# Kernel tuning notes

Measured on AMD Instinct MI355X. Metric: run time of the kernel, lower is better.

## Reference

```python
import jax, jax.numpy as jnp
import numpy as np

N, E = 50000, 800000
D_IN, D_HID, D_OUT = 128, 256, 128


def setup_inputs() -> dict:
    key = jax.random.key(0)
    k = jax.random.split(key, 7)
    x = jax.random.normal(k[0], (N, D_IN), dtype=jnp.float32)
    edge_src = jax.random.randint(k[1], (E,), 0, N, dtype=jnp.int32)
    edge_dst = jax.random.randint(k[2], (E,), 0, N, dtype=jnp.int32)
    s1 = 1.0 / np.sqrt(2 * D_IN)
    s2 = 1.0 / np.sqrt(2 * D_HID)
    W1 = jax.random.uniform(k[3], (2 * D_IN, D_HID), jnp.float32, -s1, s1)
    b1 = jax.random.uniform(k[4], (D_HID,), jnp.float32, -s1, s1)
    W2 = jax.random.uniform(k[5], (2 * D_HID, D_OUT), jnp.float32, -s2, s2)
    b2 = jax.random.uniform(k[6], (D_OUT,), jnp.float32, -s2, s2)
    return {"x": x, "edge_src": edge_src, "edge_dst": edge_dst,
            "W1": W1, "b1": b1, "W2": W2, "b2": b2}


def _sage_layer(h, edge_src, edge_dst, W, b, inv_deg):
    # mean-pool neighbor features: gather [E, D] then segment-sum to [N, D]
    msgs = h[edge_src]
    agg = jax.ops.segment_sum(msgs, edge_dst, num_segments=h.shape[0]) * inv_deg
    y = jnp.concatenate([h, agg], axis=1)  # [N, 2D]
    return y @ W + b


def reference(x, edge_src, edge_dst, W1, b1, W2, b2):
    n = x.shape[0]
    deg = jax.ops.segment_sum(jnp.ones_like(edge_dst, dtype=x.dtype), edge_dst,
                              num_segments=n)
    inv_deg = (1.0 / jnp.maximum(deg, 1.0))[:, None]  # isolated nodes -> zeros
    h = _sage_layer(x, edge_src, edge_dst, W1, b1, inv_deg)
    h = jax.nn.relu(h)
    # dropout is identity in eval mode
    h = _sage_layer(h, edge_src, edge_dst, W2, b2, inv_deg)
    return jax.nn.log_softmax(h, axis=1)
```

## Files before the change

### kernel.cpp

```cpp
#include <hip/hip_runtime.h>
#include <cstdint>
#include <cstddef>

typedef __attribute__((ext_vector_type(8))) short bf16x8;
typedef __attribute__((ext_vector_type(4))) float f32x4;
typedef __attribute__((ext_vector_type(2))) float f32x2;

__device__ inline short bf16_rne(float f) {
  unsigned u = __builtin_bit_cast(unsigned, f);
  u += 0x7fff + ((u >> 16) & 1);
  return (short)(u >> 16);
}

__device__ inline float bf16lo(unsigned v) { return __builtin_bit_cast(float, v << 16); }
__device__ inline float bf16hi(unsigned v) { return __builtin_bit_cast(float, v & 0xffff0000u); }

__device__ inline unsigned pack2(float a, float b) {
  return ((unsigned)(unsigned short)bf16_rne(a)) | (((unsigned)(unsigned short)bf16_rne(b)) << 16);
}


__global__ __launch_bounds__(256) void prep_kernel(const float* __restrict__ W1,
                                                   const float* __restrict__ W2,
                                                   const float* __restrict__ b2,
                                                   const float* __restrict__ x,
                                                   short* __restrict__ B1p,
                                                   short* __restrict__ B2p,
                                                   float* __restrict__ bias2,
                                                   unsigned* __restrict__ A1u,
                                                   unsigned* __restrict__ xf8, int nquads,
                                                   int* __restrict__ counters, int NB) {
  int b = blockIdx.x;
  int tid = threadIdx.x;
  int nqb = (nquads + 32 + 255) >> 8;
  if (b < 512) {
    int mode = b >> 8;
    int idx = (b & 255) * 256 + tid;
    int j = idx & 7;
    int L = (idx >> 3) & 63;
    int nt = (idx >> 9) & 15;
    int kb = idx >> 13;
    int k = kb * 32 + (L >> 4) * 8 + j;
    int n = nt * 16 + (L & 15);
    if (mode == 0) {
      B1p[idx] = bf16_rne(W1[(size_t)k * 256 + n]);
    } else {
      float v = (n < 128) ? W2[(size_t)k * 128 + n] : W2[(size_t)(256 + k) * 128 + (n - 128)];
      B2p[idx] = bf16_rne(v);
    }
  } else if (b == 512) {
    bias2[tid] = (tid < 128) ? b2[tid] : 0.0f;
  } else if (b < 513 + nqb) {
    int idx = (b - 513) * 256 + tid;
    if (idx < nquads) {
      int n = idx >> 5, q = idx & 31;
      float4 v = ((const float4*)x)[idx];
      ((uint2*)A1u)[(size_t)n * 64 + q] = make_uint2(pack2(v.x, v.y), pack2(v.z, v.w));
      int pk = __builtin_amdgcn_cvt_pk_fp8_f32(v.x, v.y, 0, false);
      pk = __builtin_amdgcn_cvt_pk_fp8_f32(v.z, v.w, pk, true);
      xf8[(size_t)n * 32 + q] = (unsigned)pk;
    } else if (idx < nquads + 32) {
      int n = idx >> 5, q = idx & 31;
      ((uint2*)A1u)[(size_t)n * 64 + q] = make_uint2(0u, 0u);
      xf8[(size_t)n * 32 + q] = 0u;
    }
  } else {
    for (int t = tid; t < NB; t += 256) counters[t] = 0;
  }
}

__global__ __launch_bounds__(256) void bucket_scatter(const int* __restrict__ src,
                                                      const int* __restrict__ dst, int E, int EPB,
                                                      int* __restrict__ counters, int NB,
                                                      int SLACK, unsigned* __restrict__ bedge) {
  __shared__ int h[512];
  __shared__ int base[512];
  int tid = threadIdx.x;
  for (int t = tid; t < NB; t += 256) h[t] = 0;
  __syncthreads();
  int start = blockIdx.x * EPB, end = min(E, start + EPB);
  for (int i = start + tid; i < end; i += 256) atomicAdd(&h[((unsigned)dst[i]) >> 7], 1);
  __syncthreads();
  for (int t = tid; t < NB; t += 256) {
    int c = h[t];
    base[t] = (c > 0) ? atomicAdd(&counters[t], c) : 0;
    h[t] = 0;
  }
  __syncthreads();
  for (int i = start + tid; i < end; i += 256) {
    unsigned d = (unsigned)dst[i];
    unsigned bk = d >> 7;
    int p = base[bk] + atomicAdd(&h[bk], 1);
    bedge[(size_t)bk * SLACK + p] = ((d & 127u) << 24) | (unsigned)src[i];
  }
}

__global__ __launch_bounds__(256) void build_csr(const unsigned* __restrict__ bedge,
                                                 const int* __restrict__ counters,
                                                 int NB, int SLACK, int N,
                                                 int* __restrict__ offsets,
                                                 int* __restrict__ oend,
                                                 float* __restrict__ inv_deg,
                                                 int* __restrict__ ssrc) {
  __shared__ int buf[128];
  __shared__ int cur[128];
  __shared__ int lim[128];
  int b = blockIdx.x, tid = threadIdx.x;
  int cntE = counters[b];
  int rb = b * SLACK;
  if (tid < 128) buf[tid] = 0;
  __syncthreads();
  for (int i = tid; i < cntE; i += 256) atomicAdd(&buf[bedge[(size_t)rb + i] >> 24], 1);
  __syncthreads();
  int cnt = (tid < 128) ? buf[tid] : 0;
  int pcnt = min((cnt + 3) & ~3, 64);
  if (tid < 128) buf[tid] = pcnt;
  __syncthreads();
  #pragma unroll
  for (int off = 1; off < 128; off <<= 1) {
    int t = (tid >= off && tid < 128) ? buf[tid - off] : 0;
    __syncthreads();
    if (tid < 128) buf[tid] += t;
    __syncthreads();
  }
  int excl = 0;
  if (tid < 128) {
    excl = buf[tid] - pcnt;
    int node = (b << 7) + tid;
    if (node < N) {
      offsets[node] = rb + excl;
      oend[node]    = rb + excl + pcnt;
      inv_deg[node] = 1.0f / fmaxf((float)cnt, 1.0f);
    }
  }
  __syncthreads();
  if (tid < 128) {
    cur[tid] = rb + excl;
    lim[tid] = rb + excl + pcnt;
  }
  __syncthreads();
  for (int i = tid; i < cntE; i += 256) {
    unsigned e2 = bedge[(size_t)rb + i];
    int nd = e2 >> 24;
    int p = atomicAdd(&cur[nd], 1);
    if (p < lim[nd]) ssrc[p] = (int)(e2 & 0xFFFFFFu);
  }
  __syncthreads();
  if (tid < 128) {
    int base0 = rb + excl;
    for (int p2 = cnt; p2 < pcnt; ++p2) ssrc[base0 + p2] = N;
  }
}

#define CVT8(U, A0, A1, A2, A3, A4, A5, A6, A7)                                        \
  {                                                                                    \
    f32x2 p_, q_;                                                                      \
    p_ = __builtin_amdgcn_cvt_pk_f32_fp8((U).x, false);                                \
    q_ = __builtin_amdgcn_cvt_pk_f32_fp8((U).x, true);                                 \
    A0 += p_[0]; A1 += p_[1]; A2 += q_[0]; A3 += q_[1];                                \
    p_ = __builtin_amdgcn_cvt_pk_f32_fp8((U).y, false);                                \
    q_ = __builtin_amdgcn_cvt_pk_f32_fp8((U).y, true);                                 \
    A4 += p_[0]; A5 += p_[1]; A6 += q_[0]; A7 += q_[1];                                \
  }

__global__ __launch_bounds__(256) void agg1_kernel(const uint2* __restrict__ X8,
                                                   const int* __restrict__ offsets,
                                                   const int* __restrict__ oend,
                                                   const int* __restrict__ ssrc,
                                                   const float* __restrict__ inv_deg,
                                                   uint4* __restrict__ A1q, int N) {
  int node = blockIdx.x * 4 + (threadIdx.x >> 6);
  if (node >= N) return;
  int lane = threadIdx.x & 63;
  int g = lane >> 4;
  int l = lane & 15;
  int s = offsets[node];
  int nq = (oend[node] - s) >> 2;
  int sv = ssrc[s + lane];
  float a0=0.f,a1=0.f,a2=0.f,a3=0.f,a4=0.f,a5=0.f,a6=0.f,a7=0.f;
  int q = 0;
  for (; q + 4 <= nq; q += 4) {
    int sA = __shfl(sv, (q + 0) * 4 + g, 64);
    int sB = __shfl(sv, (q + 1) * 4 + g, 64);
    int sC = __shfl(sv, (q + 2) * 4 + g, 64);
    int sD = __shfl(sv, (q + 3) * 4 + g, 64);
    uint2 u = X8[((size_t)(unsigned)sA << 4) + l];
    uint2 v = X8[((size_t)(unsigned)sB << 4) + l];
    uint2 w = X8[((size_t)(unsigned)sC << 4) + l];
    uint2 z = X8[((size_t)(unsigned)sD << 4) + l];
    CVT8(u, a0,a1,a2,a3,a4,a5,a6,a7);
    CVT8(v, a0,a1,a2,a3,a4,a5,a6,a7);
    CVT8(w, a0,a1,a2,a3,a4,a5,a6,a7);
    CVT8(z, a0,a1,a2,a3,a4,a5,a6,a7);
  }
  for (; q < nq; ++q) {
    int sA = __shfl(sv, q * 4 + g, 64);
    uint2 u = X8[((size_t)(unsigned)sA << 4) + l];
    CVT8(u, a0,a1,a2,a3,a4,a5,a6,a7);
  }
  a0 += __shfl_xor(a0,16,64); a0 += __shfl_xor(a0,32,64);
  a1 += __shfl_xor(a1,16,64); a1 += __shfl_xor(a1,32,64);
  a2 += __shfl_xor(a2,16,64); a2 += __shfl_xor(a2,32,64);
  a3 += __shfl_xor(a3,16,64); a3 += __shfl_xor(a3,32,64);
  a4 += __shfl_xor(a4,16,64); a4 += __shfl_xor(a4,32,64);
  a5 += __shfl_xor(a5,16,64); a5 += __shfl_xor(a5,32,64);
  a6 += __shfl_xor(a6,16,64); a6 += __shfl_xor(a6,32,64);
  a7 += __shfl_xor(a7,16,64); a7 += __shfl_xor(a7,32,64);
  if (g == 0) {
    float id = inv_deg[node];
    A1q[((size_t)node << 5) + 16 + l] =
        make_uint4(pack2(a0 * id, a1 * id), pack2(a2 * id, a3 * id),
                   pack2(a4 * id, a5 * id), pack2(a6 * id, a7 * id));
  }
}

__global__ __launch_bounds__(512, 2) void gemm_fused(const short* __restrict__ A,
                                                     const short* __restrict__ B1,
                                                     const short* __restrict__ B2,
                                                     const float* __restrict__ bias1,
                                                     const float* __restrict__ bias2,
                                                     short* __restrict__ utop,
                                                     unsigned char* __restrict__ t2,
                                                     int S, int Nvalid) {
  __shared__ char hls[2 * 16 * 512];
  int tid = threadIdx.x;
  int wv = tid >> 6;
  int lane = tid & 63;
  int role = wv >> 2;
  int w = wv & 3;
  int rowf = lane & 15;
  int g = lane >> 4;

  const short* Bp = role ? B2 : B1;
  const float* bias = role ? bias2 : bias1;

  bf16x8 breg[8][4];
  #pragma unroll
  for (int kb = 0; kb < 8; ++kb)
    #pragma unroll
    for (int j = 0; j < 4; ++j)
      breg[kb][j] = *(const bf16x8*)(Bp + ((size_t)((kb * 16 + w * 4 + j) * 64 + lane)) * 8);

  f32x4 bj[4];
  #pragma unroll
  for (int j = 0; j < 4; ++j)
    bj[j] = *(const f32x4*)(bias + w * 64 + j * 16 + g * 4);

  for (int i = 0;; ++i) {
    int sP = blockIdx.x + i * gridDim.x;
    int sC = blockIdx.x + (i - 1) * gridDim.x;
    bool anyP = sP < S;
    bool anyC = (i > 0) && (sC < S);
    if (!anyP && !anyC) break;

    if (role == 0) {
      if (anyP) {
        int row0 = sP * 16;
        const short* Arow = A + (size_t)(row0 + rowf) * 256 + g * 8;
        bf16x8 afr[8];
        #pragma unroll
        for (int kb = 0; kb < 8; ++kb) afr[kb] = *(const bf16x8*)(Arow + kb * 32);
        f32x4 acc[4];
        #pragma unroll
        for (int j = 0; j < 4; ++j) acc[j] = (f32x4)(0.0f);
        __builtin_amdgcn_s_setprio(1);
        #pragma unroll
        for (int kb = 0; kb < 8; ++kb)
          #pragma unroll
          for (int j = 0; j < 4; ++j)
            acc[j] = __builtin_amdgcn_mfma_f32_16x16x32_bf16(breg[kb][j], afr[kb], acc[j], 0, 0, 0);
        __builtin_amdgcn_s_setprio(0);
        int buf = (i & 1) * 8192;
        #pragma unroll
        for (int j = 0; j < 4; ++j) {
          float v0 = fmaxf(acc[j][0] + bj[j][0], 0.0f);
          float v1 = fmaxf(acc[j][1] + bj[j][1], 0.0f);
          float v2 = fmaxf(acc[j][2] + bj[j][2], 0.0f);
          float v3 = fmaxf(acc[j][3] + bj[j][3], 0.0f);
          int c0 = w * 64 + j * 16 + g * 4;
          int chunk = c0 >> 3;
          int swz = chunk ^ rowf ^ ((chunk & 1) << 4);
          *(uint2*)(hls + buf + rowf * 512 + swz * 16 + ((c0 & 4) << 1)) =
              make_uint2(pack2(v0, v1), pack2(v2, v3));
        }
      }
    } else {
      if (anyC) {
        int buf = ((i - 1) & 1) * 8192;
        bf16x8 afr[8];
        #pragma unroll
        for (int kb = 0; kb < 8; ++kb) {
          int chunk = kb * 4 + g;
          int swz = chunk ^ rowf ^ ((chunk & 1) << 4);
          afr[kb] = *(const bf16x8*)(hls + buf + rowf * 512 + swz * 16);
        }
        f32x4 acc[4];
        #pragma unroll
        for (int j = 0; j < 4; ++j) acc[j] = (f32x4)(0.0f);
        __builtin_amdgcn_s_setprio(1);
        #pragma unroll
        for (int kb = 0; kb < 8; ++kb)
          #pragma unroll
          for (int j = 0; j < 4; ++j)
            acc[j] = __builtin_amdgcn_mfma_f32_16x16x32_bf16(breg[kb][j], afr[kb], acc[j], 0, 0, 0);
        __builtin_amdgcn_s_setprio(0);
        int row = sC * 16 + rowf;
        bool live = row < Nvalid;
        #pragma unroll
        for (int j = 0; j < 4; ++j) {
          float v0 = live ? acc[j][0] + bj[j][0] : 0.0f;
          float v1 = live ? acc[j][1] + bj[j][1] : 0.0f;
          float v2 = live ? acc[j][2] + bj[j][2] : 0.0f;
          float v3 = live ? acc[j][3] + bj[j][3] : 0.0f;
          int c0 = w * 64 + j * 16 + g * 4;
          if (w < 2) {
            *(uint2*)(utop + (size_t)row * 128 + c0) = make_uint2(pack2(v0, v1), pack2(v2, v3));
          } else {
            int pk = __builtin_amdgcn_cvt_pk_fp8_f32(v0, v1, 0, false);
            pk = __builtin_amdgcn_cvt_pk_fp8_f32(v2, v3, pk, true);
            *(unsigned*)(t2 + (size_t)row * 128 + (c0 - 128)) = (unsigned)pk;
          }
        }
      }
    }
    __syncthreads();
  }
}

__global__ __launch_bounds__(256) void final_kernel(const uint4* __restrict__ utopq,
                                                    const uint2* __restrict__ T2,
                                                    const int* __restrict__ offsets,
                                                    const int* __restrict__ oend,
                                                    const int* __restrict__ ssrc,
                                                    const float* __restrict__ inv_deg,
                                                    float4* __restrict__ out4, int N) {
  int node = blockIdx.x * 4 + (threadIdx.x >> 6);
  if (node >= N) return;
  int lane = threadIdx.x & 63;
  int g = lane >> 4;
  int l = lane & 15;
  int s = offsets[node];
  int nq = (oend[node] - s) >> 2;
  int sv = ssrc[s + lane];
  float a0=0.f,a1=0.f,a2=0.f,a3=0.f,a4=0.f,a5=0.f,a6=0.f,a7=0.f;
  int q = 0;
  for (; q + 4 <= nq; q += 4) {
    int sA = __shfl(sv, (q + 0) * 4 + g, 64);
    int sB = __shfl(sv, (q + 1) * 4 + g, 64);
    int sC = __shfl(sv, (q + 2) * 4 + g, 64);
    int sD = __shfl(sv, (q + 3) * 4 + g, 64);
    uint2 u = T2[((size_t)(unsigned)sA << 4) + l];
    uint2 v = T2[((size_t)(unsigned)sB << 4) + l];
    uint2 w = T2[((size_t)(unsigned)sC << 4) + l];
    uint2 z = T2[((size_t)(unsigned)sD << 4) + l];
    CVT8(u, a0,a1,a2,a3,a4,a5,a6,a7);
    CVT8(v, a0,a1,a2,a3,a4,a5,a6,a7);
    CVT8(w, a0,a1,a2,a3,a4,a5,a6,a7);
    CVT8(z, a0,a1,a2,a3,a4,a5,a6,a7);
  }
  for (; q < nq; ++q) {
    int sA = __shfl(sv, q * 4 + g, 64);
    uint2 u = T2[((size_t)(unsigned)sA << 4) + l];
    CVT8(u, a0,a1,a2,a3,a4,a5,a6,a7);
  }
  a0 += __shfl_xor(a0,16,64); a0 += __shfl_xor(a0,32,64);
  a1 += __shfl_xor(a1,16,64); a1 += __shfl_xor(a1,32,64);
  a2 += __shfl_xor(a2,16,64); a2 += __shfl_xor(a2,32,64);
  a3 += __shfl_xor(a3,16,64); a3 += __shfl_xor(a3,32,64);
  a4 += __shfl_xor(a4,16,64); a4 += __shfl_xor(a4,32,64);
  a5 += __shfl_xor(a5,16,64); a5 += __shfl_xor(a5,32,64);
  a6 += __shfl_xor(a6,16,64); a6 += __shfl_xor(a6,32,64);
  a7 += __shfl_xor(a7,16,64); a7 += __shfl_xor(a7,32,64);
  if (g == 0) {
    float id = inv_deg[node];
    uint4 U = utopq[((size_t)node << 4) + l];
    float v0 = bf16lo(U.x) + a0 * id;
    float v1 = bf16hi(U.x) + a1 * id;
    float v2 = bf16lo(U.y) + a2 * id;
    float v3 = bf16hi(U.y) + a3 * id;
    float v4 = bf16lo(U.z) + a4 * id;
    float v5 = bf16hi(U.z) + a5 * id;
    float v6 = bf16lo(U.w) + a6 * id;
    float v7 = bf16hi(U.w) + a7 * id;
    float m = fmaxf(fmaxf(fmaxf(v0, v1), fmaxf(v2, v3)), fmaxf(fmaxf(v4, v5), fmaxf(v6, v7)));
    #pragma unroll
    for (int off = 1; off < 16; off <<= 1) m = fmaxf(m, __shfl_xor(m, off, 16));
    float su = expf(v0 - m) + expf(v1 - m) + expf(v2 - m) + expf(v3 - m) +
               expf(v4 - m) + expf(v5 - m) + expf(v6 - m) + expf(v7 - m);
    #pragma unroll
    for (int off = 1; off < 16; off <<= 1) su += __shfl_xor(su, off, 16);
    float ls = m + logf(su);
    out4[((size_t)node << 5) + l * 2]     = make_float4(v0 - ls, v1 - ls, v2 - ls, v3 - ls);
    out4[((size_t)node << 5) + l * 2 + 1] = make_float4(v4 - ls, v5 - ls, v6 - ls, v7 - ls);
  }
}

extern "C" void kernel_launch(void* const* d_in, const int* in_sizes, int n_in,
                              void* d_out, int out_size, void* d_ws, size_t ws_size,
                              hipStream_t stream) {
  const float* x        = (const float*)d_in[0];
  const int*   edge_src = (const int*)d_in[1];
  const int*   edge_dst = (const int*)d_in[2];
  const float* W1       = (const float*)d_in[3];
  const float* b1       = (const float*)d_in[4];
  const float* W2       = (const float*)d_in[5];
  const float* b2       = (const float*)d_in[6];
  float* out = (float*)d_out;

  const int D_IN = 128;
  const int N = in_sizes[0] / D_IN;
  const int E = in_sizes[1];
  const int M_pad = ((N + 128) / 128) * 128;

  const int SB = 512;
  const int EPB = (E + SB - 1) / SB;
  const int NB = (N + 127) >> 7;
  const int SLACK = 3072;

  char* ws = (char*)d_ws;
  size_t p = 0;
  auto take = [&](size_t bytes) -> size_t {
    size_t r = p;
    p += (bytes + 255) & ~(size_t)255;
    return r;
  };
  size_t cnt_off   = take((size_t)NB * 4);
  size_t bedge_off = take((size_t)NB * SLACK * 4);
  size_t offs_off  = take((size_t)N * 4);
  size_t oend_off  = take((size_t)N * 4);
  size_t inv_off   = take((size_t)N * 4);
  size_t ssrc_off  = take((size_t)NB * SLACK * 4 + 256);
  size_t A1_off    = take((size_t)M_pad * 256 * 2);
  size_t xf8_off   = take((size_t)M_pad * 128);
  size_t B1p_off   = take((size_t)256 * 256 * 2);
  size_t B2p_off   = take((size_t)256 * 256 * 2);
  size_t bias2_off = take((size_t)256 * 4);
  size_t utop_off  = take((size_t)M_pad * 128 * 2);
  size_t t2_off    = take((size_t)M_pad * 128);
  (void)ws_size;

  int*   counters = (int*)(ws + cnt_off);
  unsigned* bedge = (unsigned*)(ws + bedge_off);
  int*   offsets  = (int*)(ws + offs_off);
  int*   oendp    = (int*)(ws + oend_off);
  float* inv_deg  = (float*)(ws + inv_off);
  int*   ssrc     = (int*)(ws + ssrc_off);
  unsigned* A1u   = (unsigned*)(ws + A1_off);
  unsigned* xf8   = (unsigned*)(ws + xf8_off);
  short* B1p      = (short*)(ws + B1p_off);
  short* B2p      = (short*)(ws + B2p_off);
  float* bias2    = (float*)(ws + bias2_off);
  short* utop     = (short*)(ws + utop_off);
  unsigned char* t2f8 = (unsigned char*)(ws + t2_off);

  {
    int nquads = N * 32;
    int nqb = (nquads + 32 + 255) / 256;
    int grid = 513 + nqb + 1;
    prep_kernel<<<grid, 256, 0, stream>>>(W1, W2, b2, x, B1p, B2p, bias2, A1u, xf8, nquads,
                                          counters, NB);
  }
  bucket_scatter<<<SB, 256, 0, stream>>>(edge_src, edge_dst, E, EPB, counters, NB, SLACK, bedge);
  build_csr<<<NB, 256, 0, stream>>>(bedge, counters, NB, SLACK, N, offsets, oendp, inv_deg, ssrc);

  agg1_kernel<<<(N + 3) / 4, 256, 0, stream>>>((const uint2*)xf8, offsets, oendp, ssrc, inv_deg,
                                               (uint4*)A1u, N);
  {
    int S = M_pad / 16;
    gemm_fused<<<256, 512, 0, stream>>>((const short*)A1u, B1p, B2p, b1, bias2, utop, t2f8, S, N);
  }
  final_kernel<<<(N + 3) / 4, 256, 0, stream>>>((const uint4*)utop, (const uint2*)t2f8,
                                                offsets, oendp, ssrc, inv_deg, (float4*)out, N);
}
```

Before: 194.5 us.

## Vectorize edge bucketing, pack CSR metadata, prefetch next GEMM A tile

The edge bucketing kernel now reads dst and src as int4 vectors, and EPB is rounded to a multiple of 4 so those loads stay aligned. The CSR offsets, end pointers and inverse degree are packed into one int per node (start shifted by 8, count in the low 8 bits). The aggregation kernels decode that word and compute the inverse degree on the fly, which replaces three scattered metadata loads with one. The fused GEMM producer also prefetches the next A tile into registers after finishing the current one, to overlap the load with compute at the cost of extra register pressure. The 8-bit count field assumes degree below 256 and start offsets that fit in 24 bits.

Measured after the change: 200.5 us. 3.1% more time.

```diff
diff --git a/kernel.cpp b/kernel.cpp
--- a/kernel.cpp
+++ b/kernel.cpp
@@ -79,7 +79,15 @@
   for (int t = tid; t < NB; t += 256) h[t] = 0;
   __syncthreads();
   int start = blockIdx.x * EPB, end = min(E, start + EPB);
-  for (int i = start + tid; i < end; i += 256) atomicAdd(&h[((unsigned)dst[i]) >> 7], 1);
+  int vend = start + ((end - start) & ~3);
+  for (int i = start + tid * 4; i < vend; i += 1024) {
+    int4 d4 = *(const int4*)(dst + i);
+    atomicAdd(&h[((unsigned)d4.x) >> 7], 1);
+    atomicAdd(&h[((unsigned)d4.y) >> 7], 1);
+    atomicAdd(&h[((unsigned)d4.z) >> 7], 1);
+    atomicAdd(&h[((unsigned)d4.w) >> 7], 1);
+  }
+  for (int i = vend + tid; i < end; i += 256) atomicAdd(&h[((unsigned)dst[i]) >> 7], 1);
   __syncthreads();
   for (int t = tid; t < NB; t += 256) {
     int c = h[t];
@@ -87,7 +95,31 @@
     h[t] = 0;
   }
   __syncthreads();
-  for (int i = start + tid; i < end; i += 256) {
+  for (int i = start + tid * 4; i < vend; i += 1024) {
+    int4 d4 = *(const int4*)(dst + i);
+    int4 s4 = *(const int4*)(src + i);
+    {
+      unsigned d = (unsigned)d4.x, bk = d >> 7;
+      int p = base[bk] + atomicAdd(&h[bk], 1);
+      bedge[(size_t)bk * SLACK + p] = ((d & 127u) << 24) | (unsigned)s4.x;
+    }
+    {
+      unsigned d = (unsigned)d4.y, bk = d >> 7;
+      int p = base[bk] + atomicAdd(&h[bk], 1);
+      bedge[(size_t)bk * SLACK + p] = ((d & 127u) << 24) | (unsigned)s4.y;
+    }
+    {
+      unsigned d = (unsigned)d4.z, bk = d >> 7;
+      int p = base[bk] + atomicAdd(&h[bk], 1);
+      bedge[(size_t)bk * SLACK + p] = ((d & 127u) << 24) | (unsigned)s4.z;
+    }
+    {
+      unsigned d = (unsigned)d4.w, bk = d >> 7;
+      int p = base[bk] + atomicAdd(&h[bk], 1);
+      bedge[(size_t)bk * SLACK + p] = ((d & 127u) << 24) | (unsigned)s4.w;
+    }
+  }
+  for (int i = vend + tid; i < end; i += 256) {
     unsigned d = (unsigned)dst[i];
     unsigned bk = d >> 7;
     int p = base[bk] + atomicAdd(&h[bk], 1);
@@ -98,9 +130,7 @@
 __global__ __launch_bounds__(256) void build_csr(const unsigned* __restrict__ bedge,
                                                  const int* __restrict__ counters,
                                                  int NB, int SLACK, int N,
-                                                 int* __restrict__ offsets,
-                                                 int* __restrict__ oend,
-                                                 float* __restrict__ inv_deg,
+                                                 int* __restrict__ meta,
                                                  int* __restrict__ ssrc) {
   __shared__ int buf[128];
   __shared__ int cur[128];
@@ -127,11 +157,7 @@
   if (tid < 128) {
     excl = buf[tid] - pcnt;
     int node = (b << 7) + tid;
-    if (node < N) {
-      offsets[node] = rb + excl;
-      oend[node]    = rb + excl + pcnt;
-      inv_deg[node] = 1.0f / fmaxf((float)cnt, 1.0f);
-    }
+    if (node < N) meta[node] = ((rb + excl) << 8) | cnt;
   }
   __syncthreads();
   if (tid < 128) {
@@ -148,7 +174,7 @@
   __syncthreads();
   if (tid < 128) {
     int base0 = rb + excl;
-    for (int p2 = cnt; p2 < pcnt; ++p2) ssrc[base0 + p2] = N;
+    for (int p2 = cnt; p2 < cnt + (lim[tid] - base0 - cnt); ++p2) ssrc[base0 + p2] = N;
   }
 }
 
@@ -164,18 +190,18 @@
   }
 
 __global__ __launch_bounds__(256) void agg1_kernel(const uint2* __restrict__ X8,
-                                                   const int* __restrict__ offsets,
-                                                   const int* __restrict__ oend,
+                                                   const int* __restrict__ meta,
                                                    const int* __restrict__ ssrc,
-                                                   const float* __restrict__ inv_deg,
                                                    uint4* __restrict__ A1q, int N) {
   int node = blockIdx.x * 4 + (threadIdx.x >> 6);
   if (node >= N) return;
   int lane = threadIdx.x & 63;
   int g = lane >> 4;
   int l = lane & 15;
-  int s = offsets[node];
-  int nq = (oend[node] - s) >> 2;
+  int mv = meta[node];
+  int s = mv >> 8;
+  int cnt = mv & 255;
+  int nq = min((cnt + 3) & ~3, 64) >> 2;
   int sv = ssrc[s + lane];
   float a0=0.f,a1=0.f,a2=0.f,a3=0.f,a4=0.f,a5=0.f,a6=0.f,a7=0.f;
   int q = 0;
@@ -207,7 +233,7 @@
   a6 += __shfl_xor(a6,16,64); a6 += __shfl_xor(a6,32,64);
   a7 += __shfl_xor(a7,16,64); a7 += __shfl_xor(a7,32,64);
   if (g == 0) {
-    float id = inv_deg[node];
+    float id = 1.0f / fmaxf((float)cnt, 1.0f);
     A1q[((size_t)node << 5) + 16 + l] =
         make_uint4(pack2(a0 * id, a1 * id), pack2(a2 * id, a3 * id),
                    pack2(a4 * id, a5 * id), pack2(a6 * id, a7 * id));
@@ -246,6 +272,13 @@
   for (int j = 0; j < 4; ++j)
     bj[j] = *(const f32x4*)(bias + w * 64 + j * 16 + g * 4);
 
+  bf16x8 afr[8];
+  if (role == 0 && blockIdx.x < S) {
+    const short* Arow = A + (size_t)(blockIdx.x * 16 + rowf) * 256 + g * 8;
+    #pragma unroll
+    for (int kb = 0; kb < 8; ++kb) afr[kb] = *(const bf16x8*)(Arow + kb * 32);
+  }
+
   for (int i = 0;; ++i) {
     int sP = blockIdx.x + i * gridDim.x;
     int sC = blockIdx.x + (i - 1) * gridDim.x;
@@ -255,11 +288,6 @@
 
     if (role == 0) {
       if (anyP) {
-        int row0 = sP * 16;
-        const short* Arow = A + (size_t)(row0 + rowf) * 256 + g * 8;
-        bf16x8 afr[8];
-        #pragma unroll
-        for (int kb = 0; kb < 8; ++kb) afr[kb] = *(const bf16x8*)(Arow + kb * 32);
         f32x4 acc[4];
         #pragma unroll
         for (int j = 0; j < 4; ++j) acc[j] = (f32x4)(0.0f);
@@ -283,16 +311,22 @@
           *(uint2*)(hls + buf + rowf * 512 + swz * 16 + ((c0 & 4) << 1)) =
               make_uint2(pack2(v0, v1), pack2(v2, v3));
         }
+        int sN = sP + gridDim.x;
+        if (sN < S) {
+          const short* Arow = A + (size_t)(sN * 16 + rowf) * 256 + g * 8;
+          #pragma unroll
+          for (int kb = 0; kb < 8; ++kb) afr[kb] = *(const bf16x8*)(Arow + kb * 32);
+        }
       }
     } else {
       if (anyC) {
         int buf = ((i - 1) & 1) * 8192;
-        bf16x8 afr[8];
+        bf16x8 hfr[8];
         #pragma unroll
         for (int kb = 0; kb < 8; ++kb) {
           int chunk = kb * 4 + g;
           int swz = chunk ^ rowf ^ ((chunk & 1) << 4);
-          afr[kb] = *(const bf16x8*)(hls + buf + rowf * 512 + swz * 16);
+          hfr[kb] = *(const bf16x8*)(hls + buf + rowf * 512 + swz * 16);
         }
         f32x4 acc[4];
         #pragma unroll
@@ -302,7 +336,7 @@
         for (int kb = 0; kb < 8; ++kb)
           #pragma unroll
           for (int j = 0; j < 4; ++j)
-            acc[j] = __builtin_amdgcn_mfma_f32_16x16x32_bf16(breg[kb][j], afr[kb], acc[j], 0, 0, 0);
+            acc[j] = __builtin_amdgcn_mfma_f32_16x16x32_bf16(breg[kb][j], hfr[kb], acc[j], 0, 0, 0);
         __builtin_amdgcn_s_setprio(0);
         int row = sC * 16 + rowf;
         bool live = row < Nvalid;
@@ -329,18 +363,18 @@
 
 __global__ __launch_bounds__(256) void final_kernel(const uint4* __restrict__ utopq,
                                                     const uint2* __restrict__ T2,
-                                                    const int* __restrict__ offsets,
-                                                    const int* __restrict__ oend,
+                                                    const int* __restrict__ meta,
                                                     const int* __restrict__ ssrc,
-                                                    const float* __restrict__ inv_deg,
                                                     float4* __restrict__ out4, int N) {
   int node = blockIdx.x * 4 + (threadIdx.x >> 6);
   if (node >= N) return;
   int lane = threadIdx.x & 63;
   int g = lane >> 4;
   int l = lane & 15;
-  int s = offsets[node];
-  int nq = (oend[node] - s) >> 2;
+  int mv = meta[node];
+  int s = mv >> 8;
+  int cnt = mv & 255;
+  int nq = min((cnt + 3) & ~3, 64) >> 2;
   int sv = ssrc[s + lane];
   float a0=0.f,a1=0.f,a2=0.f,a3=0.f,a4=0.f,a5=0.f,a6=0.f,a7=0.f;
   int q = 0;
@@ -372,7 +406,7 @@
   a6 += __shfl_xor(a6,16,64); a6 += __shfl_xor(a6,32,64);
   a7 += __shfl_xor(a7,16,64); a7 += __shfl_xor(a7,32,64);
   if (g == 0) {
-    float id = inv_deg[node];
+    float id = 1.0f / fmaxf((float)cnt, 1.0f);
     uint4 U = utopq[((size_t)node << 4) + l];
     float v0 = bf16lo(U.x) + a0 * id;
     float v1 = bf16hi(U.x) + a1 * id;
@@ -413,7 +447,7 @@
   const int M_pad = ((N + 128) / 128) * 128;
 
   const int SB = 512;
-  const int EPB = (E + SB - 1) / SB;
+  const int EPB = (((E + SB - 1) / SB) + 3) & ~3;
   const int NB = (N + 127) >> 7;
   const int SLACK = 3072;
 
@@ -426,9 +460,7 @@
   };
   size_t cnt_off   = take((size_t)NB * 4);
   size_t bedge_off = take((size_t)NB * SLACK * 4);
-  size_t offs_off  = take((size_t)N * 4);
-  size_t oend_off  = take((size_t)N * 4);
-  size_t inv_off   = take((size_t)N * 4);
+  size_t meta_off  = take((size_t)N * 4);
   size_t ssrc_off  = take((size_t)NB * SLACK * 4 + 256);
   size_t A1_off    = take((size_t)M_pad * 256 * 2);
   size_t xf8_off   = take((size_t)M_pad * 128);
@@ -441,9 +473,7 @@
 
   int*   counters = (int*)(ws + cnt_off);
   unsigned* bedge = (unsigned*)(ws + bedge_off);
-  int*   offsets  = (int*)(ws + offs_off);
-  int*   oendp    = (int*)(ws + oend_off);
-  float* inv_deg  = (float*)(ws + inv_off);
+  int*   meta     = (int*)(ws + meta_off);
   int*   ssrc     = (int*)(ws + ssrc_off);
   unsigned* A1u   = (unsigned*)(ws + A1_off);
   unsigned* xf8   = (unsigned*)(ws + xf8_off);
@@ -461,14 +491,13 @@
                                           counters, NB);
   }
   bucket_scatter<<<SB, 256, 0, stream>>>(edge_src, edge_dst, E, EPB, counters, NB, SLACK, bedge);
-  build_csr<<<NB, 256, 0, stream>>>(bedge, counters, NB, SLACK, N, offsets, oendp, inv_deg, ssrc);
-
-  agg1_kernel<<<(N + 3) / 4, 256, 0, stream>>>((const uint2*)xf8, offsets, oendp, ssrc, inv_deg,
-                                               (uint4*)A1u, N);
+  build_csr<<<NB, 256, 0, stream>>>(bedge, counters, NB, SLACK, N, meta, ssrc);
+
+  agg1_kernel<<<(N + 3) / 4, 256, 0, stream>>>((const uint2*)xf8, meta, ssrc, (uint4*)A1u, N);
   {
     int S = M_pad / 16;
     gemm_fused<<<256, 512, 0, stream>>>((const short*)A1u, B1p, B2p, b1, bias2, utop, t2f8, S, N);
   }
   final_kernel<<<(N + 3) / 4, 256, 0, stream>>>((const uint4*)utop, (const uint2*)t2f8,
-                                                offsets, oendp, ssrc, inv_deg, (float4*)out, N);
-}
+                                                meta, ssrc, (float4*)out, N);
+}
```
